# Kernel optimization log

Hardware: AMD Instinct MI355X
Metric: run time of the kernel (lower is better)

## Reference

```python
import jax, jax.numpy as jnp
import numpy as np

NUM_EMBEDDINGS = 1024
EMBEDDING_DIM = 256


def setup_inputs() -> dict:
    key = jax.random.key(0)
    k1, k2 = jax.random.split(key)
    z = jax.random.normal(k1, (32, EMBEDDING_DIM, 32, 32), dtype=jnp.float32)
    codebook = jax.random.normal(k2, (NUM_EMBEDDINGS, EMBEDDING_DIM), dtype=jnp.float32)
    return {"z": z, "codebook": codebook}


def reference(z, codebook):
    # z: (B, C, H, W) -> (B, H, W, C) -> (B*H*W, C)
    B, C, H, W = z.shape
    z_bhwc = jnp.transpose(z, (0, 2, 3, 1))
    z_flat = z_bhwc.reshape(-1, C)  # (N, C)

    # pairwise squared distances: ||z||^2 + ||e||^2 - 2 z.e^T  -> (N, K)
    distances = (
        jnp.sum(z_flat ** 2, axis=1, keepdims=True)
        + jnp.sum(codebook ** 2, axis=1)
        - 2.0 * jnp.matmul(z_flat, codebook.T)
    )
    argmin_codewords = jnp.argmin(distances, axis=1)  # (N,)
    min_codewords = jax.nn.one_hot(argmin_codewords, NUM_EMBEDDINGS, dtype=jnp.float32)  # (N, K)

    # quantized latents via one-hot @ codebook, back to (B, C, H, W)
    z_quantized = jnp.matmul(min_codewords, codebook).reshape(B, H, W, C)
    z_quantized = jnp.transpose(z_quantized, (0, 3, 1, 2))
    return (min_codewords, z_quantized)
```

## Files before the change

### kernel.cpp

```cpp
#include <hip/hip_runtime.h>

#define N_ROWS 32768
#define K_CODES 1024
#define CDIM 256

typedef _Float16 half8 __attribute__((ext_vector_type(8)));
typedef _Float16 half4 __attribute__((ext_vector_type(4)));
typedef float floatx16 __attribute__((ext_vector_type(16)));
typedef unsigned long long ull;

#define WS_ZH   0ull
#define WS_ZL   16777216ull
#define WS_CBH  33554432ull
#define WS_CBL  34078720ull
#define WS_CBN  34603008ull
#define WS_PART 34607104ull
#define WS_IDX  36704256ull
#define WS_NEED 36835328ull

__device__ __forceinline__ void g2lds16(const void* g, void* l) {
    __builtin_amdgcn_global_load_lds(
        (const __attribute__((address_space(1))) void*)g,
        (__attribute__((address_space(3))) void*)l, 16, 0, 0);
}


__global__ __launch_bounds__(64) void cb_prep(const float* __restrict__ cb,
                                              _Float16* __restrict__ cbh,
                                              _Float16* __restrict__ cbl,
                                              float* __restrict__ cbn) {
    int k = blockIdx.x;
    int lane = threadIdx.x;
    float4 v = reinterpret_cast<const float4*>(cb + k * CDIM)[lane];
    float s0 = v.x * 32.f, s1 = v.y * 32.f, s2 = v.z * 32.f, s3 = v.w * 32.f;
    half4 hv, lv;
    hv[0] = (_Float16)s0; lv[0] = (_Float16)(s0 - (float)hv[0]);
    hv[1] = (_Float16)s1; lv[1] = (_Float16)(s1 - (float)hv[1]);
    hv[2] = (_Float16)s2; lv[2] = (_Float16)(s2 - (float)hv[2]);
    hv[3] = (_Float16)s3; lv[3] = (_Float16)(s3 - (float)hv[3]);
    size_t off = (size_t)((lane >> 3) * K_CODES + k) * 32 + ((lane * 4) & 31);
    *reinterpret_cast<half4*>(&cbh[off]) = hv;
    *reinterpret_cast<half4*>(&cbl[off]) = lv;
    float s = s0 * s0 + s1 * s1 + s2 * s2 + s3 * s3;
    #pragma unroll
    for (int off2 = 32; off2 > 0; off2 >>= 1) s += __shfl_down(s, off2);
    if (lane == 0) cbn[k] = s;
}

__global__ __launch_bounds__(256) void z_prep(const float* __restrict__ z,
                                              _Float16* __restrict__ zh,
                                              _Float16* __restrict__ zl) {
    __shared__ float t[64][68];
    int hwt = blockIdx.x & 15;
    int ct  = (blockIdx.x >> 4) & 3;
    int bb  = blockIdx.x >> 6;
    int tid = threadIdx.x;
    #pragma unroll
    for (int p = 0; p < 4; p++) {
        int e = p * 256 + tid;
        int c = e >> 4, h4 = e & 15;
        float4 v = *reinterpret_cast<const float4*>(
            &z[((bb * 256 + ct * 64 + c) << 10) + hwt * 64 + h4 * 4]);
        *reinterpret_cast<float4*>(&t[c][h4 * 4]) = v;
    }
    __syncthreads();
    #pragma unroll
    for (int p = 0; p < 4; p++) {
        int e = p * 256 + tid;
        int hw = e >> 4, c4 = e & 15;
        half4 hv, lv;
        #pragma unroll
        for (int j = 0; j < 4; j++) {
            float s = t[c4 * 4 + j][hw] * 32.f;
            _Float16 h = (_Float16)s;
            hv[j] = h;
            lv[j] = (_Float16)(s - (float)h);
        }
        int n = bb * 1024 + hwt * 64 + hw;
        int cg = ct * 64 + c4 * 4;
        size_t off = (size_t)((cg >> 5) * N_ROWS + n) * 32 + (cg & 31);
        *reinterpret_cast<half4*>(&zh[off]) = hv;
        *reinterpret_cast<half4*>(&zl[off]) = lv;
    }
}

__global__ __launch_bounds__(256, 3) void vq_mfma32(
    const _Float16* __restrict__ zh, const _Float16* __restrict__ zl,
    const _Float16* __restrict__ cbh, const _Float16* __restrict__ cbl,
    const float* __restrict__ cbn, ull* __restrict__ partial) {

    __shared__ _Float16 AhL[4096], AlL[4096], BhL[4096], BlL[4096];
    __shared__ float rvv[128][2];
    __shared__ int   rcc[128][2];

    const int tid = threadIdx.x;
    const int lane = tid & 63, wave = tid >> 6;
    const int wm = wave & 1, wn = wave >> 1;
    const int fm = lane & 31, fq = lane >> 5;
    const int codeTile = blockIdx.x & 7;
    const int rowTile  = blockIdx.x >> 3;
    const int rowBase = rowTile * 128, codeBase = codeTile * 128;

    floatx16 acc[4];
    #pragma unroll
    for (int i = 0; i < 4; i++) acc[i] = (floatx16)0.f;

    for (int kc = 0; kc < CDIM; kc += 32) {
        const int cc = kc >> 5;
        const size_t ab = (size_t)(cc * N_ROWS + rowBase) * 32;
        const size_t bb = (size_t)(cc * K_CODES + codeBase) * 32;
        #pragma unroll
        for (int i = 0; i < 2; i++) {
            int G = i * 256 + tid;
            int q = G >> 7, r = G & 127;
            size_t so = (size_t)r * 32 + q * 8;
            g2lds16(zh + ab + so,  &AhL[G * 8]);
            g2lds16(zl + ab + so,  &AlL[G * 8]);
            g2lds16(cbh + bb + so, &BhL[G * 8]);
            g2lds16(cbl + bb + so, &BlL[G * 8]);
        }
        __syncthreads();
        #pragma unroll
        for (int s = 0; s < 2; s++) {
            int q = s * 2 + fq;
            half8 ah[2], al[2], bh[2], bl[2];
            #pragma unroll
            for (int i = 0; i < 2; i++) {
                int ga = q * 128 + wm * 64 + i * 32 + fm;
                ah[i] = *reinterpret_cast<const half8*>(&AhL[ga * 8]);
                al[i] = *reinterpret_cast<const half8*>(&AlL[ga * 8]);
            }
            #pragma unroll
            for (int j = 0; j < 2; j++) {
                int gb = q * 128 + wn * 64 + j * 32 + fm;
                bh[j] = *reinterpret_cast<const half8*>(&BhL[gb * 8]);
                bl[j] = *reinterpret_cast<const half8*>(&BlL[gb * 8]);
            }
            #pragma unroll
            for (int i = 0; i < 2; i++)
                #pragma unroll
                for (int j = 0; j < 2; j++) {
                    acc[i*2+j] = __builtin_amdgcn_mfma_f32_32x32x16_f16(ah[i], bh[j], acc[i*2+j], 0, 0, 0);
                    acc[i*2+j] = __builtin_amdgcn_mfma_f32_32x32x16_f16(al[i], bh[j], acc[i*2+j], 0, 0, 0);
                    acc[i*2+j] = __builtin_amdgcn_mfma_f32_32x32x16_f16(ah[i], bl[j], acc[i*2+j], 0, 0, 0);
                }
        }
        __syncthreads();
    }

    float cbnv[2];
    #pragma unroll
    for (int j = 0; j < 2; j++) cbnv[j] = cbn[codeBase + wn * 64 + j * 32 + fm];

    #pragma unroll
    for (int i = 0; i < 2; i++)
        #pragma unroll
        for (int r = 0; r < 16; r++) {
            float best = 3.4e38f; int bcode = 0x7fffffff;
            #pragma unroll
            for (int j = 0; j < 2; j++) {
                float d = fmaf(-2.f, acc[i*2+j][r], cbnv[j]);
                int code = codeBase + wn * 64 + j * 32 + fm;
                if (d < best) { best = d; bcode = code; }
            }
            #pragma unroll
            for (int m = 1; m < 32; m <<= 1) {
                float ov = __shfl_xor(best, m, 64);
                int   oc = __shfl_xor(bcode, m, 64);
                if (ov < best || (ov == best && oc < bcode)) { best = ov; bcode = oc; }
            }
            if (fm == 0) {
                int row = wm * 64 + i * 32 + (r & 3) + 8 * (r >> 2) + 4 * fq;
                rvv[row][wn] = best;
                rcc[row][wn] = bcode;
            }
        }
    __syncthreads();
    if (tid < 128) {
        float v0 = rvv[tid][0]; int c0 = rcc[tid][0];
        float v1 = rvv[tid][1]; int c1 = rcc[tid][1];
        if (v1 < v0 || (v1 == v0 && c1 < c0)) { v0 = v1; c0 = c1; }
        unsigned u = __float_as_uint(v0);
        u = (u & 0x80000000u) ? ~u : (u | 0x80000000u);
        partial[(size_t)(rowBase + tid) * 8 + codeTile] =
            ((ull)u << 32) | (unsigned)c0;
    }
}

__global__ __launch_bounds__(256) void onehot_fin(const ull* __restrict__ partial,
                                                  int* __restrict__ idx,
                                                  float* __restrict__ out) {
    int row = blockIdx.x;
    __shared__ int sid;
    if (threadIdx.x < 64) {
        ull v = (threadIdx.x < 8) ? partial[(size_t)row * 8 + threadIdx.x]
                                  : ~0ull;
        #pragma unroll
        for (int m = 1; m < 8; m <<= 1) {
            ull o = __shfl_xor(v, m, 64);
            if (o < v) v = o;
        }
        if (threadIdx.x == 0) {
            int id = (int)(v & 0xffffffffu);
            sid = id;
            idx[row] = id;
        }
    }
    __syncthreads();
    int id = sid;
    int k4 = threadIdx.x << 2;
    float4 v4;
    v4.x = (k4     == id) ? 1.f : 0.f;
    v4.y = (k4 + 1 == id) ? 1.f : 0.f;
    v4.z = (k4 + 2 == id) ? 1.f : 0.f;
    v4.w = (k4 + 3 == id) ? 1.f : 0.f;
    reinterpret_cast<float4*>(out)[(size_t)row * 256 + threadIdx.x] = v4;
}

__global__ __launch_bounds__(256) void zq_fill(const int* __restrict__ idx,
                                               const float* __restrict__ cb,
                                               float* __restrict__ out) {
    int i  = blockIdx.x * 256 + threadIdx.x;
    int hw = i & 1023;
    int c  = (i >> 10) & 255;
    int b  = i >> 18;
    int n  = (b << 10) | hw;
    out[i] = cb[idx[n] * CDIM + c];
}


__global__ __launch_bounds__(64) void cb_norms(const float* __restrict__ cb,
                                               float* __restrict__ cbn) {
    int k = blockIdx.x;
    int lane = threadIdx.x;
    float4 v = reinterpret_cast<const float4*>(cb + k * CDIM)[lane];
    float s = v.x * v.x + v.y * v.y + v.z * v.z + v.w * v.w;
    #pragma unroll
    for (int off = 32; off > 0; off >>= 1) s += __shfl_down(s, off);
    if (lane == 0) cbn[k] = s;
}

__global__ __launch_bounds__(256) void cb_transpose(const float* __restrict__ cb,
                                                    float* __restrict__ cbt) {
    __shared__ float t[32][33];
    int k0 = (blockIdx.x & 31) * 32;
    int c0 = (blockIdx.x >> 5) * 32;
    int lane = threadIdx.x & 31;
    int row = threadIdx.x >> 5;
    #pragma unroll
    for (int s = 0; s < 4; s++) {
        int r = row + s * 8;
        t[r][lane] = cb[(k0 + r) * CDIM + c0 + lane];
    }
    __syncthreads();
    #pragma unroll
    for (int s = 0; s < 4; s++) {
        int r = row + s * 8;
        cbt[(c0 + r) * K_CODES + k0 + lane] = t[lane][r];
    }
}

__global__ __launch_bounds__(512, 2) void vq_argmin(const float* __restrict__ z,
                                                    const float* __restrict__ cbt,
                                                    const float* __restrict__ cbn,
                                                    int* __restrict__ idx_out) {
    __shared__ float As[64][128];
    __shared__ float Bs[64][256];

    const int tid = threadIdx.x;
    const int tx = tid & 31;
    const int ty = tid >> 5;
    const int rowBase = blockIdx.x * 128;
    const int bb = rowBase >> 10;
    const int hwBase = rowBase & 1023;

    float minv[8];
    int   mini[8];
    #pragma unroll
    for (int i = 0; i < 8; i++) { minv[i] = 3.4e38f; mini[i] = 0; }

    for (int kt = 0; kt < K_CODES; kt += 256) {
        float acc[2][2][4][4];
        #pragma unroll
        for (int a = 0; a < 2; a++)
            #pragma unroll
            for (int b = 0; b < 2; b++)
                #pragma unroll
                for (int i = 0; i < 4; i++)
                    #pragma unroll
                    for (int j = 0; j < 4; j++) acc[a][b][i][j] = 0.f;

        for (int ccb = 0; ccb < CDIM; ccb += 64) {
            #pragma unroll
            for (int l = 0; l < 4; l++) {
                int f = tid + l * 512;
                int r4 = f & 31, c = f >> 5;
                float4 v = *reinterpret_cast<const float4*>(
                    &z[((bb * 256 + ccb + c) << 10) + hwBase + r4 * 4]);
                *reinterpret_cast<float4*>(&As[c][r4 * 4]) = v;
            }
            #pragma unroll
            for (int l = 0; l < 8; l++) {
                int f = tid + l * 512;
                int k4 = f & 63, c = f >> 6;
                float4 v = *reinterpret_cast<const float4*>(
                    &cbt[(ccb + c) * K_CODES + kt + k4 * 4]);
                *reinterpret_cast<float4*>(&Bs[c][k4 * 4]) = v;
            }
            __syncthreads();
            #pragma unroll 4
            for (int c = 0; c < 64; c++) {
                float4 a0 = *reinterpret_cast<const float4*>(&As[c][ty * 4]);
                float4 a1 = *reinterpret_cast<const float4*>(&As[c][64 + ty * 4]);
                float4 b0 = *reinterpret_cast<const float4*>(&Bs[c][tx * 4]);
                float4 b1 = *reinterpret_cast<const float4*>(&Bs[c][128 + tx * 4]);
                float av[2][4] = {{a0.x, a0.y, a0.z, a0.w}, {a1.x, a1.y, a1.z, a1.w}};
                float bw[2][4] = {{b0.x, b0.y, b0.z, b0.w}, {b1.x, b1.y, b1.z, b1.w}};
                #pragma unroll
                for (int ri = 0; ri < 2; ri++)
                    #pragma unroll
                    for (int i = 0; i < 4; i++)
                        #pragma unroll
                        for (int ci = 0; ci < 2; ci++)
                            #pragma unroll
                            for (int j = 0; j < 4; j++)
                                acc[ri][ci][i][j] =
                                    fmaf(av[ri][i], bw[ci][j], acc[ri][ci][i][j]);
            }
            __syncthreads();
        }
        #pragma unroll
        for (int ci = 0; ci < 2; ci++)
            #pragma unroll
            for (int j = 0; j < 4; j++) {
                int code = kt + ci * 128 + tx * 4 + j;
                float nrm = cbn[code];
                #pragma unroll
                for (int ri = 0; ri < 2; ri++)
                    #pragma unroll
                    for (int i = 0; i < 4; i++) {
                        float d = fmaf(-2.f, acc[ri][ci][i][j], nrm);
                        int r = ri * 4 + i;
                        if (d < minv[r]) { minv[r] = d; mini[r] = code; }
                    }
            }
    }

    __syncthreads();
    float (*rv)[32] = reinterpret_cast<float(*)[32]>(&As[0][0]);
    int   (*rix)[32] = reinterpret_cast<int(*)[32]>(&As[32][0]);
    #pragma unroll
    for (int ri = 0; ri < 2; ri++)
        #pragma unroll
        for (int i = 0; i < 4; i++) {
            int row = ri * 64 + ty * 4 + i;
            rv[row][tx] = minv[ri * 4 + i];
            rix[row][tx] = mini[ri * 4 + i];
        }
    __syncthreads();
    if (tid < 128) {
        float bvv = rv[tid][0]; int bii = rix[tid][0];
        #pragma unroll
        for (int t = 1; t < 32; t++) {
            float v = rv[tid][t]; int ii = rix[tid][t];
            if (v < bvv || (v == bvv && ii < bii)) { bvv = v; bii = ii; }
        }
        idx_out[rowBase + tid] = bii;
    }
}

__global__ __launch_bounds__(256) void onehot_fill(const int* __restrict__ idx,
                                                   float* __restrict__ out) {
    int i = blockIdx.x * 256 + threadIdx.x;
    int n  = i >> 8;
    int k4 = (i & 255) << 2;
    int id = idx[n];
    float4 v;
    v.x = (k4     == id) ? 1.f : 0.f;
    v.y = (k4 + 1 == id) ? 1.f : 0.f;
    v.z = (k4 + 2 == id) ? 1.f : 0.f;
    v.w = (k4 + 3 == id) ? 1.f : 0.f;
    reinterpret_cast<float4*>(out)[i] = v;
}

extern "C" void kernel_launch(void* const* d_in, const int* in_sizes, int n_in,
                              void* d_out, int out_size, void* d_ws, size_t ws_size,
                              hipStream_t stream) {
    const float* z  = (const float*)d_in[0];
    const float* cb = (const float*)d_in[1];
    float* out0 = (float*)d_out;
    float* out1 = out0 + (size_t)N_ROWS * K_CODES;

    if (ws_size >= WS_NEED) {
        _Float16* zh  = (_Float16*)((char*)d_ws + WS_ZH);
        _Float16* zl  = (_Float16*)((char*)d_ws + WS_ZL);
        _Float16* cbh = (_Float16*)((char*)d_ws + WS_CBH);
        _Float16* cbl = (_Float16*)((char*)d_ws + WS_CBL);
        float* cbn = (float*)((char*)d_ws + WS_CBN);
        ull* part = (ull*)((char*)d_ws + WS_PART);
        int* idx = (int*)((char*)d_ws + WS_IDX);

        cb_prep<<<K_CODES, 64, 0, stream>>>(cb, cbh, cbl, cbn);
        z_prep<<<2048, 256, 0, stream>>>(z, zh, zl);
        vq_mfma32<<<2048, 256, 0, stream>>>(zh, zl, cbh, cbl, cbn, part);
        onehot_fin<<<N_ROWS, 256, 0, stream>>>(part, idx, out0);
        zq_fill<<<(N_ROWS * CDIM) / 256, 256, 0, stream>>>(idx, cb, out1);
    } else {
        float* cbn = (float*)d_ws;
        int*   idx = (int*)((char*)d_ws + 4096);
        float* cbt = (float*)((char*)d_ws + 4096 + 131072);

        cb_norms<<<K_CODES, 64, 0, stream>>>(cb, cbn);
        cb_transpose<<<256, 256, 0, stream>>>(cb, cbt);
        vq_argmin<<<N_ROWS / 128, 512, 0, stream>>>(z, cbt, cbn, idx);
        onehot_fill<<<(N_ROWS * K_CODES / 4) / 256, 256, 0, stream>>>(idx, out0);
        zq_fill<<<(N_ROWS * CDIM) / 256, 256, 0, stream>>>(idx, cb, out1);
    }
}
```

Measured before the change: 298.2 us.

## Double-buffer MFMA tile loads, merge prep kernels, batch one-hot and quantized writes

Merges the codebook and z preparation kernels into one launch. Double-buffers the LDS staging in the split-fp16 MFMA distance kernel so the next K-chunk's global-to-LDS loads overlap with the current chunk's MFMAs, with explicit vmcnt waits and raw barriers. The occupancy hint drops from 3 to 2 blocks per CU to fit the doubled LDS. The one-hot writer now handles 16 rows per block instead of 1. The quantized-output fill gathers codebook rows into shared memory and writes coalesced NCHW rows, replacing per-element gathers.

```diff
diff --git a/kernel.cpp b/kernel.cpp
--- a/kernel.cpp
+++ b/kernel.cpp
@@ -24,33 +24,33 @@
         (__attribute__((address_space(3))) void*)l, 16, 0, 0);
 }
 
-
-__global__ __launch_bounds__(64) void cb_prep(const float* __restrict__ cb,
-                                              _Float16* __restrict__ cbh,
-                                              _Float16* __restrict__ cbl,
-                                              float* __restrict__ cbn) {
-    int k = blockIdx.x;
-    int lane = threadIdx.x;
-    float4 v = reinterpret_cast<const float4*>(cb + k * CDIM)[lane];
-    float s0 = v.x * 32.f, s1 = v.y * 32.f, s2 = v.z * 32.f, s3 = v.w * 32.f;
-    half4 hv, lv;
-    hv[0] = (_Float16)s0; lv[0] = (_Float16)(s0 - (float)hv[0]);
-    hv[1] = (_Float16)s1; lv[1] = (_Float16)(s1 - (float)hv[1]);
-    hv[2] = (_Float16)s2; lv[2] = (_Float16)(s2 - (float)hv[2]);
-    hv[3] = (_Float16)s3; lv[3] = (_Float16)(s3 - (float)hv[3]);
-    size_t off = (size_t)((lane >> 3) * K_CODES + k) * 32 + ((lane * 4) & 31);
-    *reinterpret_cast<half4*>(&cbh[off]) = hv;
-    *reinterpret_cast<half4*>(&cbl[off]) = lv;
-    float s = s0 * s0 + s1 * s1 + s2 * s2 + s3 * s3;
-    #pragma unroll
-    for (int off2 = 32; off2 > 0; off2 >>= 1) s += __shfl_down(s, off2);
-    if (lane == 0) cbn[k] = s;
-}
-
-__global__ __launch_bounds__(256) void z_prep(const float* __restrict__ z,
-                                              _Float16* __restrict__ zh,
-                                              _Float16* __restrict__ zl) {
+__global__ __launch_bounds__(256) void prep_all(const float* __restrict__ z,
+                                                const float* __restrict__ cb,
+                                                _Float16* __restrict__ zh,
+                                                _Float16* __restrict__ zl,
+                                                _Float16* __restrict__ cbh,
+                                                _Float16* __restrict__ cbl,
+                                                float* __restrict__ cbn) {
     __shared__ float t[64][68];
+    if (blockIdx.x >= 2048) {
+        int k = ((blockIdx.x - 2048) << 2) | (threadIdx.x >> 6);
+        int lane = threadIdx.x & 63;
+        float4 v = reinterpret_cast<const float4*>(cb + k * CDIM)[lane];
+        float s0 = v.x * 32.f, s1 = v.y * 32.f, s2 = v.z * 32.f, s3 = v.w * 32.f;
+        half4 hv, lv;
+        hv[0] = (_Float16)s0; lv[0] = (_Float16)(s0 - (float)hv[0]);
+        hv[1] = (_Float16)s1; lv[1] = (_Float16)(s1 - (float)hv[1]);
+        hv[2] = (_Float16)s2; lv[2] = (_Float16)(s2 - (float)hv[2]);
+        hv[3] = (_Float16)s3; lv[3] = (_Float16)(s3 - (float)hv[3]);
+        size_t off = (size_t)((lane >> 3) * K_CODES + k) * 32 + ((lane * 4) & 31);
+        *reinterpret_cast<half4*>(&cbh[off]) = hv;
+        *reinterpret_cast<half4*>(&cbl[off]) = lv;
+        float s = s0 * s0 + s1 * s1 + s2 * s2 + s3 * s3;
+        #pragma unroll
+        for (int off2 = 32; off2 > 0; off2 >>= 1) s += __shfl_down(s, off2);
+        if (lane == 0) cbn[k] = s;
+        return;
+    }
     int hwt = blockIdx.x & 15;
     int ct  = (blockIdx.x >> 4) & 3;
     int bb  = blockIdx.x >> 6;
@@ -84,12 +84,13 @@
     }
 }
 
-__global__ __launch_bounds__(256, 3) void vq_mfma32(
+__global__ __launch_bounds__(256, 2) void vq_mfma32(
     const _Float16* __restrict__ zh, const _Float16* __restrict__ zl,
     const _Float16* __restrict__ cbh, const _Float16* __restrict__ cbl,
     const float* __restrict__ cbn, ull* __restrict__ partial) {
 
-    __shared__ _Float16 AhL[4096], AlL[4096], BhL[4096], BlL[4096];
+    __shared__ _Float16 AhL[2][4096], AlL[2][4096];
+    __shared__ _Float16 BhL[2][4096], BlL[2][4096];
     __shared__ float rvv[128][2];
     __shared__ int   rcc[128][2];
 
@@ -105,21 +106,31 @@
     #pragma unroll
     for (int i = 0; i < 4; i++) acc[i] = (floatx16)0.f;
 
-    for (int kc = 0; kc < CDIM; kc += 32) {
-        const int cc = kc >> 5;
-        const size_t ab = (size_t)(cc * N_ROWS + rowBase) * 32;
-        const size_t bb = (size_t)(cc * K_CODES + codeBase) * 32;
+    auto stage = [&](int buf, int ch) {
+        const size_t ab = (size_t)(ch * N_ROWS + rowBase) * 32;
+        const size_t bbo = (size_t)(ch * K_CODES + codeBase) * 32;
         #pragma unroll
         for (int i = 0; i < 2; i++) {
             int G = i * 256 + tid;
             int q = G >> 7, r = G & 127;
             size_t so = (size_t)r * 32 + q * 8;
-            g2lds16(zh + ab + so,  &AhL[G * 8]);
-            g2lds16(zl + ab + so,  &AlL[G * 8]);
-            g2lds16(cbh + bb + so, &BhL[G * 8]);
-            g2lds16(cbl + bb + so, &BlL[G * 8]);
-        }
-        __syncthreads();
+            g2lds16(zh + ab + so,  &AhL[buf][G * 8]);
+            g2lds16(zl + ab + so,  &AlL[buf][G * 8]);
+            g2lds16(cbh + bbo + so, &BhL[buf][G * 8]);
+            g2lds16(cbl + bbo + so, &BlL[buf][G * 8]);
+        }
+    };
+
+    stage(0, 0);
+    for (int c = 0; c < 8; c++) {
+        const int cur = c & 1;
+        if (c < 7) {
+            stage(cur ^ 1, c + 1);
+            asm volatile("s_waitcnt vmcnt(8)" ::: "memory");
+        } else {
+            asm volatile("s_waitcnt vmcnt(0)" ::: "memory");
+        }
+        __builtin_amdgcn_s_barrier();
         #pragma unroll
         for (int s = 0; s < 2; s++) {
             int q = s * 2 + fq;
@@ -127,14 +138,14 @@
             #pragma unroll
             for (int i = 0; i < 2; i++) {
                 int ga = q * 128 + wm * 64 + i * 32 + fm;
-                ah[i] = *reinterpret_cast<const half8*>(&AhL[ga * 8]);
-                al[i] = *reinterpret_cast<const half8*>(&AlL[ga * 8]);
+                ah[i] = *reinterpret_cast<const half8*>(&AhL[cur][ga * 8]);
+                al[i] = *reinterpret_cast<const half8*>(&AlL[cur][ga * 8]);
             }
             #pragma unroll
             for (int j = 0; j < 2; j++) {
                 int gb = q * 128 + wn * 64 + j * 32 + fm;
-                bh[j] = *reinterpret_cast<const half8*>(&BhL[gb * 8]);
-                bl[j] = *reinterpret_cast<const half8*>(&BlL[gb * 8]);
+                bh[j] = *reinterpret_cast<const half8*>(&BhL[cur][gb * 8]);
+                bl[j] = *reinterpret_cast<const half8*>(&BlL[cur][gb * 8]);
             }
             #pragma unroll
             for (int i = 0; i < 2; i++)
@@ -145,7 +156,7 @@
                     acc[i*2+j] = __builtin_amdgcn_mfma_f32_32x32x16_f16(ah[i], bl[j], acc[i*2+j], 0, 0, 0);
                 }
         }
-        __syncthreads();
+        __builtin_amdgcn_s_barrier();
     }
 
     float cbnv[2];
@@ -187,45 +198,65 @@
     }
 }
 
-__global__ __launch_bounds__(256) void onehot_fin(const ull* __restrict__ partial,
-                                                  int* __restrict__ idx,
-                                                  float* __restrict__ out) {
-    int row = blockIdx.x;
-    __shared__ int sid;
-    if (threadIdx.x < 64) {
-        ull v = (threadIdx.x < 8) ? partial[(size_t)row * 8 + threadIdx.x]
-                                  : ~0ull;
+__global__ __launch_bounds__(256) void onehot_fin2(const ull* __restrict__ partial,
+                                                   int* __restrict__ idx,
+                                                   float* __restrict__ out) {
+    __shared__ int sid[16];
+    const int rb = blockIdx.x * 16;
+    const int tid = threadIdx.x;
+    if (tid < 128) {
+        ull v = partial[(size_t)rb * 8 + tid];
         #pragma unroll
         for (int m = 1; m < 8; m <<= 1) {
             ull o = __shfl_xor(v, m, 64);
             if (o < v) v = o;
         }
-        if (threadIdx.x == 0) {
+        if ((tid & 7) == 0) {
+            int r = tid >> 3;
             int id = (int)(v & 0xffffffffu);
-            sid = id;
-            idx[row] = id;
-        }
-    }
-    __syncthreads();
-    int id = sid;
-    int k4 = threadIdx.x << 2;
-    float4 v4;
-    v4.x = (k4     == id) ? 1.f : 0.f;
-    v4.y = (k4 + 1 == id) ? 1.f : 0.f;
-    v4.z = (k4 + 2 == id) ? 1.f : 0.f;
-    v4.w = (k4 + 3 == id) ? 1.f : 0.f;
-    reinterpret_cast<float4*>(out)[(size_t)row * 256 + threadIdx.x] = v4;
-}
-
-__global__ __launch_bounds__(256) void zq_fill(const int* __restrict__ idx,
-                                               const float* __restrict__ cb,
-                                               float* __restrict__ out) {
-    int i  = blockIdx.x * 256 + threadIdx.x;
-    int hw = i & 1023;
-    int c  = (i >> 10) & 255;
-    int b  = i >> 18;
-    int n  = (b << 10) | hw;
-    out[i] = cb[idx[n] * CDIM + c];
+            sid[r] = id;
+            idx[rb + r] = id;
+        }
+    }
+    __syncthreads();
+    const int k4 = tid << 2;
+    #pragma unroll
+    for (int r = 0; r < 16; r++) {
+        int id = sid[r];
+        float4 v4;
+        v4.x = (k4     == id) ? 1.f : 0.f;
+        v4.y = (k4 + 1 == id) ? 1.f : 0.f;
+        v4.z = (k4 + 2 == id) ? 1.f : 0.f;
+        v4.w = (k4 + 3 == id) ? 1.f : 0.f;
+        reinterpret_cast<float4*>(out)[(size_t)(rb + r) * 256 + tid] = v4;
+    }
+}
+
+__global__ __launch_bounds__(256) void zq_fill2(const int* __restrict__ idx,
+                                                const float* __restrict__ cb,
+                                                float* __restrict__ out) {
+    __shared__ float tile[64][257];
+    const int tid = threadIdx.x;
+    const int n0 = (blockIdx.x >> 2) << 8;
+    const int c0 = (blockIdx.x & 3) << 6;
+    const int b  = n0 >> 10;
+    const int hw0 = n0 & 1023;
+
+    const int id = idx[n0 + tid];
+    const float4* cb4 = reinterpret_cast<const float4*>(cb);
+    #pragma unroll
+    for (int jj = 0; jj < 16; jj++) {
+        float4 v = cb4[id * 64 + (c0 >> 2) + jj];
+        tile[jj * 4 + 0][tid] = v.x;
+        tile[jj * 4 + 1][tid] = v.y;
+        tile[jj * 4 + 2][tid] = v.z;
+        tile[jj * 4 + 3][tid] = v.w;
+    }
+    __syncthreads();
+    #pragma unroll
+    for (int c = 0; c < 64; c++) {
+        out[((size_t)(b * 256 + c0 + c) << 10) + hw0 + tid] = tile[c][tid];
+    }
 }
 
 
@@ -400,11 +431,10 @@
         ull* part = (ull*)((char*)d_ws + WS_PART);
         int* idx = (int*)((char*)d_ws + WS_IDX);
 
-        cb_prep<<<K_CODES, 64, 0, stream>>>(cb, cbh, cbl, cbn);
-        z_prep<<<2048, 256, 0, stream>>>(z, zh, zl);
+        prep_all<<<2304, 256, 0, stream>>>(z, cb, zh, zl, cbh, cbl, cbn);
         vq_mfma32<<<2048, 256, 0, stream>>>(zh, zl, cbh, cbl, cbn, part);
-        onehot_fin<<<N_ROWS, 256, 0, stream>>>(part, idx, out0);
-        zq_fill<<<(N_ROWS * CDIM) / 256, 256, 0, stream>>>(idx, cb, out1);
+        onehot_fin2<<<2048, 256, 0, stream>>>(part, idx, out0);
+        zq_fill2<<<512, 256, 0, stream>>>(idx, cb, out1);
     } else {
         float* cbn = (float*)d_ws;
         int*   idx = (int*)((char*)d_ws + 4096);
@@ -414,6 +444,6 @@
         cb_transpose<<<256, 256, 0, stream>>>(cb, cbt);
         vq_argmin<<<N_ROWS / 128, 512, 0, stream>>>(z, cbt, cbn, idx);
         onehot_fill<<<(N_ROWS * K_CODES / 4) / 256, 256, 0, stream>>>(idx, out0);
-        zq_fill<<<(N_ROWS * CDIM) / 256, 256, 0, stream>>>(idx, cb, out1);
-    }
-}
+        zq_fill2<<<512, 256, 0, stream>>>(idx, cb, out1);
+    }
+}
```

Measured after the change: 313.1 us. 5.0% more time.
